# Kernel optimization log

Hardware: AMD Instinct MI355X
Metric: run time of the kernel (lower is better)

The kernel has to match this reference:

```python
import jax, jax.numpy as jnp
import numpy as np

DD = 2.5
GAMMA = 0.005


def setup_inputs() -> dict:
    key = jax.random.key(0)
    k1, k2 = jax.random.split(key)
    B, C, H, W = 8, 32, 512, 512
    K = 16
    features_batch = jax.random.normal(k1, (B, C, H, W), dtype=jnp.float32)
    labels_batch = jax.random.randint(k2, (B, H, W), 0, K, dtype=jnp.int64)
    return {"features_batch": features_batch, "labels_batch": labels_batch, "num_instances": K}


def _per_image_loss(f, lab, K):
    # f: [N, C], lab: [N] int in [0, K)
    counts = jax.ops.segment_sum(jnp.ones(lab.shape, f.dtype), lab, num_segments=K)  # [K]
    sums = jax.ops.segment_sum(f, lab, num_segments=K)                               # [K, C]
    means = sums / counts[:, None]                                                   # [K, C]
    # variance term: mean over pixels of ||x - mean_cluster||^2, summed over clusters
    d2 = jnp.sum((f - means[lab]) ** 2, axis=1)                                      # [N]
    var_loss = jnp.sum(jax.ops.segment_sum(d2, lab, num_segments=K) / counts)
    # pairwise hinge distance term over i<j
    diff2 = jnp.sum((means[:, None, :] - means[None, :, :]) ** 2, axis=-1)           # [K, K]
    eye = jnp.eye(K, dtype=bool)
    dist = jnp.sqrt(jnp.where(eye, 1.0, diff2))  # safe sqrt on diagonal
    hinge = jnp.maximum(2.0 * DD - dist, 0.0) ** 2
    pair_mask = jnp.triu(jnp.ones((K, K), dtype=bool), k=1)
    dist_loss = jnp.sum(jnp.where(pair_mask, hinge, 0.0)) / (K - 1)
    # regularizer: sum of L2 norms of cluster means
    reg_loss = jnp.sum(jnp.sqrt(jnp.sum(means ** 2, axis=-1)))
    return (var_loss + dist_loss + GAMMA * reg_loss) / K


def reference(features_batch, labels_batch, num_instances):
    B, C, H, W = features_batch.shape
    K = int(num_instances)
    feats = jnp.transpose(features_batch, (0, 2, 3, 1)).reshape(B, H * W, C)
    labs = labels_batch.reshape(B, H * W)
    losses = jax.vmap(lambda f, l: _per_image_loss(f, l, K))(feats, labs)  # [B]
    return jnp.sum(losses) / (B + 1)
```

## Files before the change

### kernel.cpp

```cpp
#include <hip/hip_runtime.h>

#define NPIX (512*512)
#define KCL 16
#define IMG_STRIDE 1088
#define ZERO_BYTES (8 * IMG_STRIDE * 4)

typedef __attribute__((ext_vector_type(8))) short bf16x8;
typedef __attribute__((ext_vector_type(4))) float f32x4;
typedef __attribute__((ext_vector_type(4))) int i32x4;

static __device__ __forceinline__ unsigned int bf16rne(float x) {
  unsigned int u = __builtin_bit_cast(unsigned int, x);
  u += 0x7FFFu + ((u >> 16) & 1u);
  return u >> 16;
}
static __device__ __forceinline__ int pk2(float a, float b) {
  return (int)(bf16rne(a) | (bf16rne(b) << 16));
}

#define RS_LEVEL(ARR, HALF, MASK) { \
    const bool hi = (lane & (MASK)) != 0; \
    _Pragma("unroll") \
    for (int j = 0; j < (HALF); ++j) { \
      float send = hi ? ARR[j] : ARR[j + (HALF)]; \
      float recv = __shfl_xor(send, (MASK), 64); \
      ARR[j] = (hi ? ARR[j + (HALF)] : ARR[j]) + recv; \
    } }

__global__ void __launch_bounds__(512)
cl_accum(const float* __restrict__ feats, const int* __restrict__ labs,
         float* __restrict__ ws)
{
  const int bid  = blockIdx.x;
  const int tile = bid & 63;
  const int b    = bid >> 6;
  const int tid  = threadIdx.x;
  const int wave = tid >> 6;
  const int lane = tid & 63;
  const int px0  = tile * 4096;

  __shared__ unsigned int slabw[1024];
  __shared__ float red[1024];
  __shared__ float hpart[8][KCL];

  {
    float c[KCL];
    #pragma unroll
    for (int k = 0; k < KCL; ++k) c[k] = 0.f;
    const int4* lb4 = reinterpret_cast<const int4*>(labs + b * NPIX + px0);
    #pragma unroll
    for (int i = 0; i < 2; ++i) {
      const int4 v = lb4[tid + i * 512];
      slabw[tid + i * 512] = (unsigned int)v.x | ((unsigned int)v.y << 8) |
                             ((unsigned int)v.z << 16) | ((unsigned int)v.w << 24);
      #pragma unroll
      for (int k = 0; k < KCL; ++k) {
        c[k] += (v.x == k) ? 1.0f : 0.0f;
        c[k] += (v.y == k) ? 1.0f : 0.0f;
        c[k] += (v.z == k) ? 1.0f : 0.0f;
        c[k] += (v.w == k) ? 1.0f : 0.0f;
      }
    }
    red[tid] = 0.f;
    red[tid + 512] = 0.f;
    RS_LEVEL(c, 8, 1)
    RS_LEVEL(c, 4, 2)
    RS_LEVEL(c, 2, 4)
    RS_LEVEL(c, 1, 8)
    c[0] += __shfl_xor(c[0], 16, 64);
    c[0] += __shfl_xor(c[0], 32, 64);
    if (lane < KCL) {
      const int v4 = (int)(__brev((unsigned)lane) >> 28);
      hpart[wave][v4] = c[0];
    }
  }
  __syncthreads();
  if (tid < KCL) {
    float t = 0.f;
    #pragma unroll
    for (int w = 0; w < 8; ++w) t += hpart[w][tid];
    atomicAdd(&ws[b * IMG_STRIDE + tid], t);
  }

  const int kid = lane & 15;
  const int sub = lane >> 4;
  const float* fA = feats + ((long long)(b * 32 + kid)) * NPIX
                    + px0 + wave * 512 + sub * 8;
  const float* fB = fA + (long long)16 * NPIX;
  const unsigned long long* slq =
      reinterpret_cast<const unsigned long long*>(slabw) + wave * 64 + sub;

  f32x4 accs0 = {0.f, 0.f, 0.f, 0.f};
  f32x4 accs1 = {0.f, 0.f, 0.f, 0.f};
  f32x4 accq0 = {0.f, 0.f, 0.f, 0.f};
  f32x4 accq1 = {0.f, 0.f, 0.f, 0.f};

  #pragma unroll 4
  for (int g = 0; g < 16; ++g) {
    const unsigned long long lw = slq[g * 4];
    bf16x8 af;
    #pragma unroll
    for (int j = 0; j < 8; ++j)
      af[j] = (short)((((int)(lw >> (8 * j)) & 0xFF) == kid) ? 0x3F80 : 0);

    {
      const float4 x0 = *reinterpret_cast<const float4*>(fA + g * 32);
      const float4 x1 = *reinterpret_cast<const float4*>(fA + g * 32 + 4);
      i32x4 wv, qv;
      wv[0] = pk2(x0.x, x0.y); wv[1] = pk2(x0.z, x0.w);
      wv[2] = pk2(x1.x, x1.y); wv[3] = pk2(x1.z, x1.w);
      qv[0] = pk2(x0.x * x0.x, x0.y * x0.y); qv[1] = pk2(x0.z * x0.z, x0.w * x0.w);
      qv[2] = pk2(x1.x * x1.x, x1.y * x1.y); qv[3] = pk2(x1.z * x1.z, x1.w * x1.w);
      accs0 = __builtin_amdgcn_mfma_f32_16x16x32_bf16(
                  af, __builtin_bit_cast(bf16x8, wv), accs0, 0, 0, 0);
      accq0 = __builtin_amdgcn_mfma_f32_16x16x32_bf16(
                  af, __builtin_bit_cast(bf16x8, qv), accq0, 0, 0, 0);
    }
    {
      const float4 x0 = *reinterpret_cast<const float4*>(fB + g * 32);
      const float4 x1 = *reinterpret_cast<const float4*>(fB + g * 32 + 4);
      i32x4 wv, qv;
      wv[0] = pk2(x0.x, x0.y); wv[1] = pk2(x0.z, x0.w);
      wv[2] = pk2(x1.x, x1.y); wv[3] = pk2(x1.z, x1.w);
      qv[0] = pk2(x0.x * x0.x, x0.y * x0.y); qv[1] = pk2(x0.z * x0.z, x0.w * x0.w);
      qv[2] = pk2(x1.x * x1.x, x1.y * x1.y); qv[3] = pk2(x1.z * x1.z, x1.w * x1.w);
      accs1 = __builtin_amdgcn_mfma_f32_16x16x32_bf16(
                  af, __builtin_bit_cast(bf16x8, wv), accs1, 0, 0, 0);
      accq1 = __builtin_amdgcn_mfma_f32_16x16x32_bf16(
                  af, __builtin_bit_cast(bf16x8, qv), accq1, 0, 0, 0);
    }
  }

  #pragma unroll
  for (int r = 0; r < 4; ++r) {
    const int k = sub * 4 + r;
    atomicAdd(&red[k * 32 + kid],            accs0[r]);
    atomicAdd(&red[k * 32 + 16 + kid],       accs1[r]);
    atomicAdd(&red[512 + k * 32 + kid],      accq0[r]);
    atomicAdd(&red[512 + k * 32 + 16 + kid], accq1[r]);
  }
  __syncthreads();
  atomicAdd(&ws[b * IMG_STRIDE + 32 + tid],  red[tid]);
  atomicAdd(&ws[b * IMG_STRIDE + 544 + tid], red[512 + tid]);
}

__global__ void __launch_bounds__(512)
cl_finalize(const float* __restrict__ ws, float* __restrict__ out)
{
  __shared__ float smean[8][KCL][33];
  __shared__ float slossb[8];
  const int tid  = threadIdx.x;
  const int w    = tid >> 6;
  const int lane = tid & 63;
  const float* base = ws + w * IMG_STRIDE;

  const int kl = lane >> 2;
  const float ik = 1.0f / base[kl];

  float m2part = 0.f, sqpart = 0.f;
  #pragma unroll
  for (int j = 0; j < 8; ++j) {
    const int idx = lane * 8 + j;
    const int c = idx & 31;
    const float m = base[32 + idx] * ik;
    smean[w][kl][c] = m;
    m2part = fmaf(m, m, m2part);
    sqpart += base[544 + idx];
  }
  float varp = fmaf(sqpart, ik, -m2part);
  #pragma unroll
  for (int mk = 1; mk < 64; mk <<= 1) varp += __shfl_xor(varp, mk, 64);

  __syncthreads();

  const int kk = lane >> 2, q = lane & 3;
  float n2 = 0.f;
  #pragma unroll
  for (int j = 0; j < 8; ++j) {
    const float m = smean[w][kk][q * 8 + j];
    n2 = fmaf(m, m, n2);
  }
  n2 += __shfl_xor(n2, 1, 64);
  n2 += __shfl_xor(n2, 2, 64);
  float regp = (q == 0) ? sqrtf(n2) : 0.f;
  #pragma unroll
  for (int mk = 1; mk < 64; mk <<= 1) regp += __shfl_xor(regp, mk, 64);

  float hing = 0.f;
  for (int p = lane; p < 120; p += 64) {
    int i = 0, rem = p;
    while (rem >= 15 - i) { rem -= 15 - i; ++i; }
    const int jj = i + 1 + rem;
    float d2 = 0.f;
    #pragma unroll
    for (int c = 0; c < 32; ++c) {
      const float d = smean[w][i][c] - smean[w][jj][c];
      d2 = fmaf(d, d, d2);
    }
    const float h = fmaxf(5.0f - sqrtf(d2), 0.f);
    hing = fmaf(h, h, hing);
  }
  #pragma unroll
  for (int mk = 1; mk < 64; mk <<= 1) hing += __shfl_xor(hing, mk, 64);

  if (lane == 0)
    slossb[w] = (varp + hing * (1.0f / 15.0f) + 0.005f * regp) * (1.0f / 16.0f);
  __syncthreads();
  if (tid == 0) {
    float t = 0.f;
    #pragma unroll
    for (int i = 0; i < 8; ++i) t += slossb[i];
    out[0] = t * (1.0f / 9.0f);
  }
}

extern "C" void kernel_launch(void* const* d_in, const int* in_sizes, int n_in,
                              void* d_out, int out_size, void* d_ws, size_t ws_size,
                              hipStream_t stream)
{
  const float* feats = (const float*)d_in[0];
  const int*   labs  = (const int*)d_in[1];
  float* out = (float*)d_out;
  float* ws  = (float*)d_ws;

  (void)hipMemsetAsync(d_ws, 0, ZERO_BYTES, stream);
  hipLaunchKernelGGL(cl_accum,    dim3(512), dim3(512), 0, stream, feats, labs, ws);
  hipLaunchKernelGGL(cl_finalize, dim3(1),   dim3(512), 0, stream, ws, out);
}
```

Before: 68.85 us.

## Split label packing into prep kernel and stage features through double-buffered LDS

Adds a prep kernel that counts labels and packs them to bytes in workspace, so the accumulate kernel reads 1-byte labels instead of 4-byte ints. The accumulate kernel now splits channels into 4 groups of 8 per block and loads coalesced float4 rows per channel into a double-buffered shared-memory tile, with register prefetch of the next chunk. Half of the MFMA lanes now feed zeros because only 8 channels are processed, which wastes matrix throughput. Adds an extra launch, two barriers per iteration, and label traffic that is read four times across channel groups.

```diff
diff --git a/kernel.cpp b/kernel.cpp
--- a/kernel.cpp
+++ b/kernel.cpp
@@ -3,7 +3,8 @@
 #define NPIX (512*512)
 #define KCL 16
 #define IMG_STRIDE 1088
-#define ZERO_BYTES (8 * IMG_STRIDE * 4)
+#define LAB_OFF 8704
+#define ZERO_BYTES (LAB_OFF * 4)
 
 typedef __attribute__((ext_vector_type(8))) short bf16x8;
 typedef __attribute__((ext_vector_type(4))) float f32x4;
@@ -28,120 +29,140 @@
     } }
 
 __global__ void __launch_bounds__(512)
-cl_accum(const float* __restrict__ feats, const int* __restrict__ labs,
-         float* __restrict__ ws)
+cl_prep(const int* __restrict__ labs, float* __restrict__ ws)
+{
+  const int b    = blockIdx.x >> 4;
+  const int seg  = blockIdx.x & 15;
+  const int tid  = threadIdx.x;
+  const int lane = tid & 63;
+  const int4* lb4 = reinterpret_cast<const int4*>(labs + b * NPIX + seg * 16384);
+  unsigned int* lab8 = reinterpret_cast<unsigned int*>(ws + LAB_OFF) +
+                       (b * NPIX + seg * 16384) / 4;
+
+  float c[KCL];
+  #pragma unroll
+  for (int k = 0; k < KCL; ++k) c[k] = 0.f;
+  #pragma unroll
+  for (int i = 0; i < 8; ++i) {
+    const int4 v = lb4[tid + i * 512];
+    lab8[tid + i * 512] = (unsigned int)(v.x & 15) | ((unsigned int)(v.y & 15) << 8) |
+                          ((unsigned int)(v.z & 15) << 16) | ((unsigned int)(v.w & 15) << 24);
+    #pragma unroll
+    for (int k = 0; k < KCL; ++k) {
+      c[k] += (v.x == k) ? 1.0f : 0.0f;
+      c[k] += (v.y == k) ? 1.0f : 0.0f;
+      c[k] += (v.z == k) ? 1.0f : 0.0f;
+      c[k] += (v.w == k) ? 1.0f : 0.0f;
+    }
+  }
+  RS_LEVEL(c, 8, 1)
+  RS_LEVEL(c, 4, 2)
+  RS_LEVEL(c, 2, 4)
+  RS_LEVEL(c, 1, 8)
+  c[0] += __shfl_xor(c[0], 16, 64);
+  c[0] += __shfl_xor(c[0], 32, 64);
+  if (lane < KCL) {
+    const int v4 = (int)(__brev((unsigned)lane) >> 28);
+    atomicAdd(&ws[b * IMG_STRIDE + v4], c[0]);
+  }
+}
+
+__global__ void __launch_bounds__(512)
+cl_accum(const float* __restrict__ feats, float* __restrict__ ws)
 {
   const int bid  = blockIdx.x;
-  const int tile = bid & 63;
+  const int pt   = bid & 15;
+  const int cg   = (bid >> 4) & 3;
   const int b    = bid >> 6;
   const int tid  = threadIdx.x;
   const int wave = tid >> 6;
   const int lane = tid & 63;
-  const int px0  = tile * 4096;
-
-  __shared__ unsigned int slabw[1024];
-  __shared__ float red[1024];
-  __shared__ float hpart[8][KCL];
-
-  {
-    float c[KCL];
-    #pragma unroll
-    for (int k = 0; k < KCL; ++k) c[k] = 0.f;
-    const int4* lb4 = reinterpret_cast<const int4*>(labs + b * NPIX + px0);
-    #pragma unroll
-    for (int i = 0; i < 2; ++i) {
-      const int4 v = lb4[tid + i * 512];
-      slabw[tid + i * 512] = (unsigned int)v.x | ((unsigned int)v.y << 8) |
-                             ((unsigned int)v.z << 16) | ((unsigned int)v.w << 24);
+  const int kid  = lane & 15;
+  const int sub  = lane >> 4;
+  const int px0  = pt * 16384;
+
+  __shared__ float sfeat[2][8][1028];
+  __shared__ float red[256];
+
+  if (tid < 256) red[tid] = 0.f;
+
+  const float* fptr = feats + ((long long)(b * 32 + cg * 8 + wave)) * NPIX + px0;
+  const unsigned long long* lab64 = reinterpret_cast<const unsigned long long*>(
+      reinterpret_cast<const unsigned char*>(ws) + (size_t)ZERO_BYTES + (size_t)b * NPIX + px0);
+
+  f32x4 accs = {0.f, 0.f, 0.f, 0.f};
+  f32x4 accq = {0.f, 0.f, 0.f, 0.f};
+
+  float4 pf0, pf1, pf2, pf3;
+  pf0 = *reinterpret_cast<const float4*>(fptr + lane * 4);
+  pf1 = *reinterpret_cast<const float4*>(fptr + 256 + lane * 4);
+  pf2 = *reinterpret_cast<const float4*>(fptr + 512 + lane * 4);
+  pf3 = *reinterpret_cast<const float4*>(fptr + 768 + lane * 4);
+  *reinterpret_cast<float4*>(&sfeat[0][wave][lane * 4])       = pf0;
+  *reinterpret_cast<float4*>(&sfeat[0][wave][256 + lane * 4]) = pf1;
+  *reinterpret_cast<float4*>(&sfeat[0][wave][512 + lane * 4]) = pf2;
+  *reinterpret_cast<float4*>(&sfeat[0][wave][768 + lane * 4]) = pf3;
+  __syncthreads();
+
+  for (int r = 0; r < 16; ++r) {
+    const int cur = r & 1, nxt = cur ^ 1;
+    if (r < 15) {
+      const float* np = fptr + (r + 1) * 1024;
+      pf0 = *reinterpret_cast<const float4*>(np + lane * 4);
+      pf1 = *reinterpret_cast<const float4*>(np + 256 + lane * 4);
+      pf2 = *reinterpret_cast<const float4*>(np + 512 + lane * 4);
+      pf3 = *reinterpret_cast<const float4*>(np + 768 + lane * 4);
+    }
+
+    #pragma unroll
+    for (int g2 = 0; g2 < 4; ++g2) {
+      const unsigned long long lw = lab64[r * 128 + wave * 16 + g2 * 4 + sub];
+      bf16x8 af;
       #pragma unroll
-      for (int k = 0; k < KCL; ++k) {
-        c[k] += (v.x == k) ? 1.0f : 0.0f;
-        c[k] += (v.y == k) ? 1.0f : 0.0f;
-        c[k] += (v.z == k) ? 1.0f : 0.0f;
-        c[k] += (v.w == k) ? 1.0f : 0.0f;
+      for (int j = 0; j < 8; ++j)
+        af[j] = (short)((((int)(lw >> (8 * j)) & 0xFF) == kid) ? 0x3F80 : 0);
+
+      i32x4 wv = {0, 0, 0, 0}, qv = {0, 0, 0, 0};
+      if (kid < 8) {
+        const float* rp = &sfeat[cur][kid][wave * 128 + g2 * 32 + sub * 8];
+        const float4 x0 = *reinterpret_cast<const float4*>(rp);
+        const float4 x1 = *reinterpret_cast<const float4*>(rp + 4);
+        wv[0] = pk2(x0.x, x0.y); wv[1] = pk2(x0.z, x0.w);
+        wv[2] = pk2(x1.x, x1.y); wv[3] = pk2(x1.z, x1.w);
+        qv[0] = pk2(x0.x * x0.x, x0.y * x0.y); qv[1] = pk2(x0.z * x0.z, x0.w * x0.w);
+        qv[2] = pk2(x1.x * x1.x, x1.y * x1.y); qv[3] = pk2(x1.z * x1.z, x1.w * x1.w);
       }
-    }
-    red[tid] = 0.f;
-    red[tid + 512] = 0.f;
-    RS_LEVEL(c, 8, 1)
-    RS_LEVEL(c, 4, 2)
-    RS_LEVEL(c, 2, 4)
-    RS_LEVEL(c, 1, 8)
-    c[0] += __shfl_xor(c[0], 16, 64);
-    c[0] += __shfl_xor(c[0], 32, 64);
-    if (lane < KCL) {
-      const int v4 = (int)(__brev((unsigned)lane) >> 28);
-      hpart[wave][v4] = c[0];
-    }
-  }
-  __syncthreads();
-  if (tid < KCL) {
-    float t = 0.f;
-    #pragma unroll
-    for (int w = 0; w < 8; ++w) t += hpart[w][tid];
-    atomicAdd(&ws[b * IMG_STRIDE + tid], t);
-  }
-
-  const int kid = lane & 15;
-  const int sub = lane >> 4;
-  const float* fA = feats + ((long long)(b * 32 + kid)) * NPIX
-                    + px0 + wave * 512 + sub * 8;
-  const float* fB = fA + (long long)16 * NPIX;
-  const unsigned long long* slq =
-      reinterpret_cast<const unsigned long long*>(slabw) + wave * 64 + sub;
-
-  f32x4 accs0 = {0.f, 0.f, 0.f, 0.f};
-  f32x4 accs1 = {0.f, 0.f, 0.f, 0.f};
-  f32x4 accq0 = {0.f, 0.f, 0.f, 0.f};
-  f32x4 accq1 = {0.f, 0.f, 0.f, 0.f};
-
-  #pragma unroll 4
-  for (int g = 0; g < 16; ++g) {
-    const unsigned long long lw = slq[g * 4];
-    bf16x8 af;
-    #pragma unroll
-    for (int j = 0; j < 8; ++j)
-      af[j] = (short)((((int)(lw >> (8 * j)) & 0xFF) == kid) ? 0x3F80 : 0);
-
-    {
-      const float4 x0 = *reinterpret_cast<const float4*>(fA + g * 32);
-      const float4 x1 = *reinterpret_cast<const float4*>(fA + g * 32 + 4);
-      i32x4 wv, qv;
-      wv[0] = pk2(x0.x, x0.y); wv[1] = pk2(x0.z, x0.w);
-      wv[2] = pk2(x1.x, x1.y); wv[3] = pk2(x1.z, x1.w);
-      qv[0] = pk2(x0.x * x0.x, x0.y * x0.y); qv[1] = pk2(x0.z * x0.z, x0.w * x0.w);
-      qv[2] = pk2(x1.x * x1.x, x1.y * x1.y); qv[3] = pk2(x1.z * x1.z, x1.w * x1.w);
-      accs0 = __builtin_amdgcn_mfma_f32_16x16x32_bf16(
-                  af, __builtin_bit_cast(bf16x8, wv), accs0, 0, 0, 0);
-      accq0 = __builtin_amdgcn_mfma_f32_16x16x32_bf16(
-                  af, __builtin_bit_cast(bf16x8, qv), accq0, 0, 0, 0);
-    }
-    {
-      const float4 x0 = *reinterpret_cast<const float4*>(fB + g * 32);
-      const float4 x1 = *reinterpret_cast<const float4*>(fB + g * 32 + 4);
-      i32x4 wv, qv;
-      wv[0] = pk2(x0.x, x0.y); wv[1] = pk2(x0.z, x0.w);
-      wv[2] = pk2(x1.x, x1.y); wv[3] = pk2(x1.z, x1.w);
-      qv[0] = pk2(x0.x * x0.x, x0.y * x0.y); qv[1] = pk2(x0.z * x0.z, x0.w * x0.w);
-      qv[2] = pk2(x1.x * x1.x, x1.y * x1.y); qv[3] = pk2(x1.z * x1.z, x1.w * x1.w);
-      accs1 = __builtin_amdgcn_mfma_f32_16x16x32_bf16(
-                  af, __builtin_bit_cast(bf16x8, wv), accs1, 0, 0, 0);
-      accq1 = __builtin_amdgcn_mfma_f32_16x16x32_bf16(
-                  af, __builtin_bit_cast(bf16x8, qv), accq1, 0, 0, 0);
-    }
-  }
-
-  #pragma unroll
-  for (int r = 0; r < 4; ++r) {
-    const int k = sub * 4 + r;
-    atomicAdd(&red[k * 32 + kid],            accs0[r]);
-    atomicAdd(&red[k * 32 + 16 + kid],       accs1[r]);
-    atomicAdd(&red[512 + k * 32 + kid],      accq0[r]);
-    atomicAdd(&red[512 + k * 32 + 16 + kid], accq1[r]);
-  }
-  __syncthreads();
-  atomicAdd(&ws[b * IMG_STRIDE + 32 + tid],  red[tid]);
-  atomicAdd(&ws[b * IMG_STRIDE + 544 + tid], red[512 + tid]);
+      accs = __builtin_amdgcn_mfma_f32_16x16x32_bf16(
+                 af, __builtin_bit_cast(bf16x8, wv), accs, 0, 0, 0);
+      accq = __builtin_amdgcn_mfma_f32_16x16x32_bf16(
+                 af, __builtin_bit_cast(bf16x8, qv), accq, 0, 0, 0);
+    }
+    __syncthreads();
+
+    if (r < 15) {
+      *reinterpret_cast<float4*>(&sfeat[nxt][wave][lane * 4])       = pf0;
+      *reinterpret_cast<float4*>(&sfeat[nxt][wave][256 + lane * 4]) = pf1;
+      *reinterpret_cast<float4*>(&sfeat[nxt][wave][512 + lane * 4]) = pf2;
+      *reinterpret_cast<float4*>(&sfeat[nxt][wave][768 + lane * 4]) = pf3;
+    }
+    __syncthreads();
+  }
+
+  if (kid < 8) {
+    #pragma unroll
+    for (int rr = 0; rr < 4; ++rr) {
+      const int k = sub * 4 + rr;
+      atomicAdd(&red[k * 8 + kid],       accs[rr]);
+      atomicAdd(&red[128 + k * 8 + kid], accq[rr]);
+    }
+  }
+  __syncthreads();
+  if (tid < 128) {
+    const int k  = tid >> 3;
+    const int ch = (tid & 7) + cg * 8;
+    atomicAdd(&ws[b * IMG_STRIDE + 32  + k * 32 + ch], red[tid]);
+    atomicAdd(&ws[b * IMG_STRIDE + 544 + k * 32 + ch], red[128 + tid]);
+  }
 }
 
 __global__ void __launch_bounds__(512)
@@ -224,6 +245,7 @@
   float* ws  = (float*)d_ws;
 
   (void)hipMemsetAsync(d_ws, 0, ZERO_BYTES, stream);
-  hipLaunchKernelGGL(cl_accum,    dim3(512), dim3(512), 0, stream, feats, labs, ws);
+  hipLaunchKernelGGL(cl_prep,     dim3(128), dim3(512), 0, stream, labs, ws);
+  hipLaunchKernelGGL(cl_accum,    dim3(512), dim3(512), 0, stream, feats, ws);
   hipLaunchKernelGGL(cl_finalize, dim3(1),   dim3(512), 0, stream, ws, out);
 }
```

Measured after the change: 86.28 us. +25.3%, slower.

## Coalesce feature loads across lanes, stagger tile order, use nontemporal loads

Applied to the files above, without the earlier changes.

Changes the pixel-to-lane mapping so the four sub-groups of a channel read adjacent 16-byte chunks, making each wave's feature load one contiguous 64-byte segment per channel instead of strided 32-byte pieces. Label words are fetched as two 32-bit LDS reads matching the new mapping. The iteration order is rotated per wave and tile to spread DRAM access across channels. Feature reads are marked nontemporal to avoid polluting the cache with streamed data.

```diff
diff --git a/kernel.cpp b/kernel.cpp
--- a/kernel.cpp
+++ b/kernel.cpp
@@ -85,10 +85,9 @@
   const int kid = lane & 15;
   const int sub = lane >> 4;
   const float* fA = feats + ((long long)(b * 32 + kid)) * NPIX
-                    + px0 + wave * 512 + sub * 8;
+                    + px0 + wave * 512 + sub * 4;
   const float* fB = fA + (long long)16 * NPIX;
-  const unsigned long long* slq =
-      reinterpret_cast<const unsigned long long*>(slabw) + wave * 64 + sub;
+  const int lwbase = wave * 128;
 
   f32x4 accs0 = {0.f, 0.f, 0.f, 0.f};
   f32x4 accs1 = {0.f, 0.f, 0.f, 0.f};
@@ -96,34 +95,42 @@
   f32x4 accq1 = {0.f, 0.f, 0.f, 0.f};
 
   #pragma unroll 4
-  for (int g = 0; g < 16; ++g) {
-    const unsigned long long lw = slq[g * 4];
+  for (int g0 = 0; g0 < 16; ++g0) {
+    const int g = (g0 + wave * 2 + tile) & 15;
+    const unsigned int l0 = slabw[lwbase + g * 8 + sub];
+    const unsigned int l1 = slabw[lwbase + g * 8 + 4 + sub];
     bf16x8 af;
     #pragma unroll
-    for (int j = 0; j < 8; ++j)
-      af[j] = (short)((((int)(lw >> (8 * j)) & 0xFF) == kid) ? 0x3F80 : 0);
+    for (int j = 0; j < 4; ++j) {
+      af[j]     = (short)((((int)(l0 >> (8 * j)) & 0xFF) == kid) ? 0x3F80 : 0);
+      af[4 + j] = (short)((((int)(l1 >> (8 * j)) & 0xFF) == kid) ? 0x3F80 : 0);
+    }
 
     {
-      const float4 x0 = *reinterpret_cast<const float4*>(fA + g * 32);
-      const float4 x1 = *reinterpret_cast<const float4*>(fA + g * 32 + 4);
+      const f32x4 x0 = __builtin_nontemporal_load(
+          reinterpret_cast<const f32x4*>(fA + g * 32));
+      const f32x4 x1 = __builtin_nontemporal_load(
+          reinterpret_cast<const f32x4*>(fA + g * 32 + 16));
       i32x4 wv, qv;
-      wv[0] = pk2(x0.x, x0.y); wv[1] = pk2(x0.z, x0.w);
-      wv[2] = pk2(x1.x, x1.y); wv[3] = pk2(x1.z, x1.w);
-      qv[0] = pk2(x0.x * x0.x, x0.y * x0.y); qv[1] = pk2(x0.z * x0.z, x0.w * x0.w);
-      qv[2] = pk2(x1.x * x1.x, x1.y * x1.y); qv[3] = pk2(x1.z * x1.z, x1.w * x1.w);
+      wv[0] = pk2(x0[0], x0[1]); wv[1] = pk2(x0[2], x0[3]);
+      wv[2] = pk2(x1[0], x1[1]); wv[3] = pk2(x1[2], x1[3]);
+      qv[0] = pk2(x0[0] * x0[0], x0[1] * x0[1]); qv[1] = pk2(x0[2] * x0[2], x0[3] * x0[3]);
+      qv[2] = pk2(x1[0] * x1[0], x1[1] * x1[1]); qv[3] = pk2(x1[2] * x1[2], x1[3] * x1[3]);
       accs0 = __builtin_amdgcn_mfma_f32_16x16x32_bf16(
                   af, __builtin_bit_cast(bf16x8, wv), accs0, 0, 0, 0);
       accq0 = __builtin_amdgcn_mfma_f32_16x16x32_bf16(
                   af, __builtin_bit_cast(bf16x8, qv), accq0, 0, 0, 0);
     }
     {
-      const float4 x0 = *reinterpret_cast<const float4*>(fB + g * 32);
-      const float4 x1 = *reinterpret_cast<const float4*>(fB + g * 32 + 4);
+      const f32x4 x0 = __builtin_nontemporal_load(
+          reinterpret_cast<const f32x4*>(fB + g * 32));
+      const f32x4 x1 = __builtin_nontemporal_load(
+          reinterpret_cast<const f32x4*>(fB + g * 32 + 16));
       i32x4 wv, qv;
-      wv[0] = pk2(x0.x, x0.y); wv[1] = pk2(x0.z, x0.w);
-      wv[2] = pk2(x1.x, x1.y); wv[3] = pk2(x1.z, x1.w);
-      qv[0] = pk2(x0.x * x0.x, x0.y * x0.y); qv[1] = pk2(x0.z * x0.z, x0.w * x0.w);
-      qv[2] = pk2(x1.x * x1.x, x1.y * x1.y); qv[3] = pk2(x1.z * x1.z, x1.w * x1.w);
+      wv[0] = pk2(x0[0], x0[1]); wv[1] = pk2(x0[2], x0[3]);
+      wv[2] = pk2(x1[0], x1[1]); wv[3] = pk2(x1[2], x1[3]);
+      qv[0] = pk2(x0[0] * x0[0], x0[1] * x0[1]); qv[1] = pk2(x0[2] * x0[2], x0[3] * x0[3]);
+      qv[2] = pk2(x1[0] * x1[0], x1[1] * x1[1]); qv[3] = pk2(x1[2] * x1[2], x1[3] * x1[3]);
       accs1 = __builtin_amdgcn_mfma_f32_16x16x32_bf16(
                   af, __builtin_bit_cast(bf16x8, wv), accs1, 0, 0, 0);
       accq1 = __builtin_amdgcn_mfma_f32_16x16x32_bf16(
```

After: 83.54 us. +21.3%, slower.
